# Kernel optimization log

Measured on AMD Instinct MI355X. Metric: run time of the kernel, lower is better.

## Reference

```python
import jax, jax.numpy as jnp
import numpy as np

NUM_HEADS = 8
OUT_FEATS = 64
TOPK_T = 10          # settings['T']
NEG_INF = -9e15

N_NODES = 8192
IN_FEATS = 512
N_EDGES = 262144  # avg degree 32


def setup_inputs() -> dict:
    key = jax.random.key(0)
    k1, k2, k3, k4, k5 = jax.random.split(key, 5)
    feat = jax.random.normal(k1, (N_NODES, IN_FEATS), jnp.float32)
    # xavier-ish scale for the fc weight [H*D, in_feats]
    fc_weight = jax.random.normal(k2, (NUM_HEADS * OUT_FEATS, IN_FEATS), jnp.float32) * 0.05
    trans_m = jax.random.uniform(k3, (N_EDGES,), jnp.float32)
    src = jax.random.randint(k4, (N_EDGES,), 0, N_NODES, dtype=jnp.int32)
    dst = jax.random.randint(k5, (N_EDGES,), 0, N_NODES, dtype=jnp.int32)
    return {"feat": feat, "fc_weight": fc_weight, "trans_m": trans_m, "src": src, "dst": dst}


def reference(feat, fc_weight, trans_m, src, dst):
    N = feat.shape[0]
    # fc projection -> [N, H, D]
    feat_src = (feat @ fc_weight.T).reshape(N, NUM_HEADS, OUT_FEATS)
    # per-edge per-head dot-product score (SDDMM; same math as the gathered NxN matmul)
    fs, fd = feat_src[src], feat_src[dst]           # [Ne, H, D]
    e = jnp.einsum('ehd,ehd->eh', fs, fd)           # [Ne, H]
    # sparse attn values = sum over heads of e * trans_m, scattered into dense [N, N]
    vals = (e * trans_m[:, None]).sum(-1)           # [Ne]
    attn_dense = jnp.zeros((N, N), feat.dtype).at[src, dst].add(vals)
    # topk mask per row: threshold = clamp(kth largest, min=0); below -> -9e15
    thresh = jnp.maximum(jax.lax.top_k(attn_dense, TOPK_T)[0][:, -1], 0.0)  # [N]
    masked = jnp.where(attn_dense < thresh[:, None], NEG_INF, attn_dense)
    # attn = masked.T ; gather attn[src, dst] == masked[dst, src]; mask edges where < -100
    cond = masked[dst, src] < -100.0                # [Ne]
    e = jnp.where(cond[:, None], NEG_INF, e)
    # edge_softmax over incoming edges of each dst node
    emax = jax.ops.segment_max(e, dst, num_segments=N)        # [N, H]
    e_exp = jnp.exp(e - emax[dst])                            # [Ne, H]
    esum = jax.ops.segment_sum(e_exp, dst, num_segments=N)    # [N, H]
    a = e_exp / esum[dst]                                     # [Ne, H]
    # u_mul_e + sum aggregation: rst[v] = sum_{(u,v) in E} a * feat_src[u]
    rst = jax.ops.segment_sum(a[:, :, None] * fs, dst, num_segments=N)  # [N, H, D]
    return rst
```

## Files before the change

kernel.cpp:

```cpp
#include <hip/hip_runtime.h>
#include <hip/hip_bf16.h>
#include <math.h>

#define N_NODES 8192
#define IN_FEATS 512
#define N_EDGES 262144
#define NUM_HEADS 8
#define OUT_FEATS 64
#define HD (NUM_HEADS * OUT_FEATS)
#define TOPK 10
#define NEG_INF -9e15f
#define MAXD 128
#define EID_MASK 0x3FFFF

__device__ __forceinline__ int swz(int row, int k4) {
  return k4 ^ (4 * (((row & 7) ^ ((row >> 3) & 7)) & 7));
}

__global__ __launch_bounds__(512, 2) void gemm_nt(const float* __restrict__ A,
                                                  const float* __restrict__ B,
                                                  float* __restrict__ C,
                                                  ushort* __restrict__ C16) {
  __shared__ char smem[65536];
  int tid = threadIdx.x;
  int sub = tid >> 8;
  int stid = tid & 255;
  int tx = stid & 15, ty = stid >> 4;
  int brow = blockIdx.x * 128, bcol = blockIdx.y * 128;
  int kbase = sub * 256;

  float (*Asub)[32] = (float(*)[32])(smem + sub * 16384);
  float (*Bsub)[32] = (float(*)[32])(smem + 32768 + sub * 16384);

  int sr = stid >> 1;
  int skc = (stid & 1) * 8;
  const float* gA = A + (size_t)(brow + sr) * IN_FEATS + kbase + skc;
  const float* gB = B + (size_t)(bcol + sr) * IN_FEATS + kbase + skc;
  int w0 = swz(sr, skc), w1 = swz(sr, skc + 4);

  float acc[8][8];
#pragma unroll
  for (int i = 0; i < 8; i++)
#pragma unroll
    for (int j = 0; j < 8; j++) acc[i][j] = 0.f;

  float4 ra0 = *(const float4*)gA;
  float4 ra1 = *(const float4*)(gA + 4);
  float4 rb0 = *(const float4*)gB;
  float4 rb1 = *(const float4*)(gB + 4);

  const int NT = 16;
  for (int t = 0; t < NT; ++t) {
    __syncthreads();
    *(float4*)&Asub[sr][w0] = ra0; *(float4*)&Asub[sr][w1] = ra1;
    *(float4*)&Bsub[sr][w0] = rb0; *(float4*)&Bsub[sr][w1] = rb1;
    if (t + 1 < NT) {
      const float* pA = gA + (t + 1) * 16;
      const float* pB = gB + (t + 1) * 16;
      ra0 = *(const float4*)pA; ra1 = *(const float4*)(pA + 4);
      rb0 = *(const float4*)pB; rb1 = *(const float4*)(pB + 4);
    }
    __syncthreads();
#pragma unroll
    for (int g = 0; g < 4; ++g) {
      float4 av[8], bv[8];
#pragma unroll
      for (int i = 0; i < 8; i++) {
        int r = ty * 8 + i;
        av[i] = *(const float4*)&Asub[r][swz(r, g * 4)];
      }
#pragma unroll
      for (int j = 0; j < 8; j++) {
        int c = tx * 8 + j;
        bv[j] = *(const float4*)&Bsub[c][swz(c, g * 4)];
      }
#pragma unroll
      for (int i = 0; i < 8; i++)
#pragma unroll
        for (int j = 0; j < 8; j++) {
          acc[i][j] = fmaf(av[i].x, bv[j].x, acc[i][j]);
          acc[i][j] = fmaf(av[i].y, bv[j].y, acc[i][j]);
          acc[i][j] = fmaf(av[i].z, bv[j].z, acc[i][j]);
          acc[i][j] = fmaf(av[i].w, bv[j].w, acc[i][j]);
        }
    }
  }

  float (*xch)[33] = (float(*)[33])smem;
  __syncthreads();
#pragma unroll
  for (int r = 0; r < 2; ++r) {
    if (sub == 1) {
#pragma unroll
      for (int k = 0; k < 32; ++k) {
        int idx = r * 32 + k;
        xch[stid][k] = acc[idx >> 3][idx & 7];
      }
    }
    __syncthreads();
    if (sub == 0) {
#pragma unroll
      for (int k = 0; k < 32; ++k) {
        int idx = r * 32 + k;
        acc[idx >> 3][idx & 7] += xch[stid][k];
      }
    }
    __syncthreads();
  }

  if (sub == 0) {
#pragma unroll
    for (int i = 0; i < 8; i++) {
      int row = brow + ty * 8 + i;
      float* cp = C + (size_t)row * HD + bcol + tx * 8;
      *(float4*)cp = make_float4(acc[i][0], acc[i][1], acc[i][2], acc[i][3]);
      *(float4*)(cp + 4) = make_float4(acc[i][4], acc[i][5], acc[i][6], acc[i][7]);
      ushort u[8];
#pragma unroll
      for (int j = 0; j < 8; j++) u[j] = __bfloat16_as_ushort(__float2bfloat16(acc[i][j]));
      uint4 q;
      q.x = (unsigned)u[0] | ((unsigned)u[1] << 16);
      q.y = (unsigned)u[2] | ((unsigned)u[3] << 16);
      q.z = (unsigned)u[4] | ((unsigned)u[5] << 16);
      q.w = (unsigned)u[6] | ((unsigned)u[7] << 16);
      *(uint4*)(C16 + (size_t)row * HD + bcol + tx * 8) = q;
    }
  }
}

__global__ __launch_bounds__(256) void histo(const int* __restrict__ src, const int* __restrict__ dst,
                                             int* __restrict__ cnt_s, int* __restrict__ cnt_d) {
  int e = blockIdx.x * blockDim.x + threadIdx.x;
  if (e < N_EDGES) {
    atomicAdd(&cnt_s[src[e]], 1);
    atomicAdd(&cnt_d[dst[e]], 1);
  }
}

__global__ __launch_bounds__(1024) void scan2(const int* __restrict__ cnt_s, const int* __restrict__ cnt_d,
                                              int* __restrict__ rp_s, int* __restrict__ rp_d) {
  __shared__ int ls[1024];
  const int* cnt = blockIdx.x ? cnt_d : cnt_s;
  int* rp = blockIdx.x ? rp_d : rp_s;
  int t = threadIdx.x;
  int base = t * 8;
  int v[8]; int s = 0;
#pragma unroll
  for (int i = 0; i < 8; i++) { v[i] = cnt[base + i]; s += v[i]; }
  ls[t] = s;
  __syncthreads();
  for (int off = 1; off < 1024; off <<= 1) {
    int x = (t >= off) ? ls[t - off] : 0;
    __syncthreads();
    ls[t] += x;
    __syncthreads();
  }
  int excl = (t == 0) ? 0 : ls[t - 1];
#pragma unroll
  for (int i = 0; i < 8; i++) { rp[base + i] = excl; excl += v[i]; }
  if (t == 1023) rp[N_NODES] = excl;
}

__global__ __launch_bounds__(256) void scatter_csr(const int* __restrict__ src, const int* __restrict__ dst,
                                                   const int* __restrict__ rp_s, const int* __restrict__ rp_d,
                                                   int* __restrict__ fill_s, int* __restrict__ fill_d,
                                                   int* __restrict__ cs, int* __restrict__ cd) {
  int e = blockIdx.x * blockDim.x + threadIdx.x;
  if (e < N_EDGES) {
    int p = rp_s[src[e]] + atomicAdd(&fill_s[src[e]], 1);
    cs[p] = e;
    int q = rp_d[dst[e]] + atomicAdd(&fill_d[dst[e]], 1);
    cd[q] = e;
  }
}

__global__ __launch_bounds__(256) void sort_rows_bitonic(const int* __restrict__ rp_s,
                                                         const int* __restrict__ rp_d,
                                                         const int* __restrict__ dst,
                                                         int* __restrict__ cs, int* __restrict__ cd,
                                                         int* __restrict__ keys_s) {
  int wave = (blockIdx.x * blockDim.x + threadIdx.x) >> 6;
  int lane = threadIdx.x & 63;
  bool is_s = wave < N_NODES;
  int r = is_s ? wave : wave - N_NODES;
  const int* rp = is_s ? rp_s : rp_d;
  int b = rp[r], e2 = rp[r + 1];
  int len = e2 - b; if (len > 128) len = 128;

  int x0 = 0x7FFFFFFF, x1 = 0x7FFFFFFF;
  if (lane < len) {
    int e = is_s ? cs[b + lane] : cd[b + lane];
    x0 = is_s ? ((dst[e] << 18) | e) : e;
  }
  if (lane + 64 < len) {
    int e = is_s ? cs[b + lane + 64] : cd[b + lane + 64];
    x1 = is_s ? ((dst[e] << 18) | e) : e;
  }

  for (int s = 2; s <= 64; s <<= 1) {
    bool asc1 = ((64 & s) == 0);
    for (int d = s >> 1; d >= 1; d >>= 1) {
      {
        int y = __shfl_xor(x0, d);
        bool keepmin = (((lane & d) == 0) == ((lane & s) == 0));
        x0 = keepmin ? min(x0, y) : max(x0, y);
      }
      {
        int y = __shfl_xor(x1, d);
        bool asc = asc1 ? ((lane & s) == 0) : false;
        bool keepmin = (((lane & d) == 0) == asc);
        x1 = keepmin ? min(x1, y) : max(x1, y);
      }
    }
  }
  { int lo = min(x0, x1), hi = max(x0, x1); x0 = lo; x1 = hi; }
  for (int d = 32; d >= 1; d >>= 1) {
    {
      int y = __shfl_xor(x0, d);
      bool keepmin = ((lane & d) == 0);
      x0 = keepmin ? min(x0, y) : max(x0, y);
    }
    {
      int y = __shfl_xor(x1, d);
      bool keepmin = ((lane & d) == 0);
      x1 = keepmin ? min(x1, y) : max(x1, y);
    }
  }

  if (lane < len) {
    if (is_s) { cs[b + lane] = x0 & EID_MASK; keys_s[b + lane] = x0; }
    else cd[b + lane] = x0;
  }
  if (lane + 64 < len) {
    if (is_s) { cs[b + lane + 64] = x1 & EID_MASK; keys_s[b + lane + 64] = x1; }
    else cd[b + lane + 64] = x1;
  }
}

__global__ __launch_bounds__(256) void edge_scores_row(const float* __restrict__ fsrc,
                                                       const int* __restrict__ dst,
                                                       const float* __restrict__ trans,
                                                       const int* __restrict__ rp_s,
                                                       const int* __restrict__ cs,
                                                       float* __restrict__ escore, float* __restrict__ val) {
  int wave = (blockIdx.x * blockDim.x + threadIdx.x) >> 6;
  int lane = threadIdx.x & 63;
  if (wave >= N_NODES) return;
  int b = rp_s[wave], e2 = rp_s[wave + 1];
  if (b == e2) return;
  const float4* ps = (const float4*)(fsrc + (size_t)wave * HD) + lane * 2;
  float4 s0 = ps[0], s1 = ps[1];
  int head = lane >> 3;
  bool leader = (lane & 7) == 0;
  for (int i = b; i < e2; i++) {
    int e = cs[i];
    int d = dst[e];
    const float4* pd = (const float4*)(fsrc + (size_t)d * HD) + lane * 2;
    float4 d0 = pd[0], d1 = pd[1];
    float dot = s0.x * d0.x + s0.y * d0.y + s0.z * d0.z + s0.w * d0.w
              + s1.x * d1.x + s1.y * d1.y + s1.z * d1.z + s1.w * d1.w;
    dot += __shfl_xor(dot, 1);
    dot += __shfl_xor(dot, 2);
    dot += __shfl_xor(dot, 4);
    if (leader) escore[(size_t)e * 8 + head] = dot;
    float x = leader ? dot * trans[e] : 0.f;
    x += __shfl_xor(x, 8);
    x += __shfl_xor(x, 16);
    x += __shfl_xor(x, 32);
    if (lane == 0) val[e] = x;
  }
}

__global__ __launch_bounds__(256) void topk_wave(const int* __restrict__ rp_s,
                                                 const int* __restrict__ keys_s,
                                                 const float* __restrict__ val,
                                                 float* __restrict__ aval,
                                                 float* __restrict__ thresh) {
  int wave = (blockIdx.x * blockDim.x + threadIdx.x) >> 6;
  int lane = threadIdx.x & 63;
  if (wave >= N_NODES) return;
  int b = rp_s[wave], e2 = rp_s[wave + 1];
  int len = e2 - b; if (len > 128) len = 128;
  float c[2];
#pragma unroll
  for (int k = 0; k < 2; k++) {
    int i = lane + 64 * k;
    float cv = 0.f;
    if (i < len) {
      int key = keys_s[b + i];
      int d = key >> 18;
      int prevd = (i == 0) ? -1 : (keys_s[b + i - 1] >> 18);
      if (d != prevd) {
        float s = val[key & EID_MASK];
        for (int j = i + 1; j < len; j++) {
          int kj = keys_s[b + j];
          if ((kj >> 18) != d) break;
          s += val[kj & EID_MASK];
        }
        cv = s;
        aval[b + i] = s;
      } else {
        aval[b + i] = 0.f;
      }
    }
    c[k] = cv;
  }
  float t10 = 0.f;
  for (int t = 0; t < 10; t++) {
    float m = fmaxf(c[0], c[1]);
#pragma unroll
    for (int off = 1; off < 64; off <<= 1) m = fmaxf(m, __shfl_xor(m, off));
    if (m <= 0.f) { t10 = 0.f; break; }
    t10 = m;
    if (t == 9) break;
    unsigned long long b0 = __ballot(c[0] == m);
    if (b0) {
      int l = __ffsll(b0) - 1;
      if (lane == l) c[0] = -1e30f;
    } else {
      unsigned long long b1 = __ballot(c[1] == m);
      int l = __ffsll(b1) - 1;
      if (lane == l) c[1] = -1e30f;
    }
  }
  if (lane == 0) thresh[wave] = fmaxf(t10, 0.f);
}

__global__ __launch_bounds__(256) void cond_edges(const int* __restrict__ src, const int* __restrict__ dst,
                                                  const int* __restrict__ rp_s,
                                                  const int* __restrict__ keys_s,
                                                  const float* __restrict__ aval,
                                                  const float* __restrict__ thresh,
                                                  unsigned char* __restrict__ cond) {
  int e = blockIdx.x * blockDim.x + threadIdx.x;
  if (e >= N_EDGES) return;
  int s = src[e], d = dst[e];
  int lo = rp_s[d], hi = rp_s[d + 1];
  int end = hi;
  int target = s << 18;
  while (lo < hi) {
    int mid = (lo + hi) >> 1;
    if (keys_s[mid] < target) lo = mid + 1; else hi = mid;
  }
  float a = 0.f;
  if (lo < end && (keys_s[lo] >> 18) == s) a = aval[lo];
  cond[e] = (a < thresh[d]) ? 1 : 0;
}

__global__ __launch_bounds__(64) void dst_softmax_agg(const int* __restrict__ rp_d, const int* __restrict__ cd,
                                                      const int* __restrict__ src,
                                                      const unsigned char* __restrict__ cond,
                                                      const float* __restrict__ escore,
                                                      const ushort* __restrict__ fsrc16,
                                                      float* __restrict__ out) {
  __shared__ float p_lds[MAXD * 9];
  __shared__ int u_lds[MAXD];
  int v = blockIdx.x;
  int lane = threadIdx.x;
  int rb = rp_d[v], re = rp_d[v + 1];
  int d = re - rb;
  if (d > MAXD) d = MAXD;

  float sc[2][8];
  float m[8];
#pragma unroll
  for (int h = 0; h < 8; h++) m[h] = -3.0e38f;

#pragma unroll
  for (int k = 0; k < 2; k++) {
    int il = lane + 64 * k;
    if (il < d) {
      int ei = cd[rb + il];
      int u = src[ei];
      u_lds[il] = u;
      bool cmask = cond[ei] != 0;
      const float* sp = escore + (size_t)ei * 8;
      float4 s0 = *(const float4*)sp;
      float4 s1 = *(const float4*)(sp + 4);
      float ss[8] = {s0.x, s0.y, s0.z, s0.w, s1.x, s1.y, s1.z, s1.w};
#pragma unroll
      for (int h = 0; h < 8; h++) {
        float x = cmask ? NEG_INF : ss[h];
        sc[k][h] = x;
        m[h] = fmaxf(m[h], x);
      }
    } else {
#pragma unroll
      for (int h = 0; h < 8; h++) sc[k][h] = -3.0e38f;
    }
  }
#pragma unroll
  for (int off = 1; off < 64; off <<= 1)
#pragma unroll
    for (int h = 0; h < 8; h++) m[h] = fmaxf(m[h], __shfl_xor(m[h], off));

  float z[8];
#pragma unroll
  for (int h = 0; h < 8; h++) z[h] = 0.f;
#pragma unroll
  for (int k = 0; k < 2; k++) {
    int il = lane + 64 * k;
    if (il < d) {
#pragma unroll
      for (int h = 0; h < 8; h++) {
        float p = expf(sc[k][h] - m[h]);
        z[h] += p;
        p_lds[il * 9 + h] = p;
      }
    }
  }
#pragma unroll
  for (int off = 1; off < 64; off <<= 1)
#pragma unroll
    for (int h = 0; h < 8; h++) z[h] += __shfl_xor(z[h], off);

  int myh = lane >> 3;
  float zh = 0.f;
#pragma unroll
  for (int h = 0; h < 8; h++) zh = (h == myh) ? z[h] : zh;
  float invZ = (d > 0) ? (1.0f / zh) : 0.f;

  __syncthreads();

  float acc[8];
#pragma unroll
  for (int j = 0; j < 8; j++) acc[j] = 0.f;
  for (int i = 0; i < d; i++) {
    float w = p_lds[i * 9 + myh] * invZ;
    const ushort* fp = fsrc16 + (size_t)u_lds[i] * HD + lane * 8;
    uint4 q = *(const uint4*)fp;
    acc[0] = fmaf(w, __uint_as_float(q.x << 16), acc[0]);
    acc[1] = fmaf(w, __uint_as_float(q.x & 0xFFFF0000u), acc[1]);
    acc[2] = fmaf(w, __uint_as_float(q.y << 16), acc[2]);
    acc[3] = fmaf(w, __uint_as_float(q.y & 0xFFFF0000u), acc[3]);
    acc[4] = fmaf(w, __uint_as_float(q.z << 16), acc[4]);
    acc[5] = fmaf(w, __uint_as_float(q.z & 0xFFFF0000u), acc[5]);
    acc[6] = fmaf(w, __uint_as_float(q.w << 16), acc[6]);
    acc[7] = fmaf(w, __uint_as_float(q.w & 0xFFFF0000u), acc[7]);
  }
  float* op = out + (size_t)v * HD + lane * 8;
  *(float4*)op = make_float4(acc[0], acc[1], acc[2], acc[3]);
  *(float4*)(op + 4) = make_float4(acc[4], acc[5], acc[6], acc[7]);
}

extern "C" void kernel_launch(void* const* d_in, const int* in_sizes, int n_in,
                              void* d_out, int out_size, void* d_ws, size_t ws_size,
                              hipStream_t stream) {
  const float* feat = (const float*)d_in[0];
  const float* fcw = (const float*)d_in[1];
  const float* trans = (const float*)d_in[2];
  const int* src = (const int*)d_in[3];
  const int* dst = (const int*)d_in[4];
  float* out = (float*)d_out;

  char* ws = (char*)d_ws;
  size_t off = 0;
  auto alloc = [&](size_t bytes) -> void* {
    size_t o = off;
    off = (off + bytes + 255) & ~(size_t)255;
    return (void*)(ws + o);
  };
  float* fsrc = (float*)alloc((size_t)N_NODES * HD * 4);
  ushort* fsrc16 = (ushort*)alloc((size_t)N_NODES * HD * 2);
  float* escore = (float*)alloc((size_t)N_EDGES * 8 * 4);
  float* val = (float*)alloc((size_t)N_EDGES * 4);
  int* cnt = (int*)alloc((size_t)4 * N_NODES * 4);
  int* rp_s = (int*)alloc((size_t)(N_NODES + 1) * 4);
  int* rp_d = (int*)alloc((size_t)(N_NODES + 1) * 4);
  int* cs = (int*)alloc((size_t)N_EDGES * 4);
  int* cd = (int*)alloc((size_t)N_EDGES * 4);
  int* keys_s = (int*)alloc((size_t)N_EDGES * 4);
  float* aval = (float*)alloc((size_t)N_EDGES * 4);
  float* thresh = (float*)alloc((size_t)N_NODES * 4);
  unsigned char* cond = (unsigned char*)alloc((size_t)N_EDGES);
  if (off > ws_size) return;

  int* cnt_s = cnt;
  int* cnt_d = cnt + N_NODES;
  int* fill_s = cnt + 2 * N_NODES;
  int* fill_d = cnt + 3 * N_NODES;

  hipMemsetAsync(cnt, 0, (size_t)4 * N_NODES * 4, stream);
  histo<<<N_EDGES / 256, 256, 0, stream>>>(src, dst, cnt_s, cnt_d);
  scan2<<<2, 1024, 0, stream>>>(cnt_s, cnt_d, rp_s, rp_d);
  scatter_csr<<<N_EDGES / 256, 256, 0, stream>>>(src, dst, rp_s, rp_d, fill_s, fill_d, cs, cd);
  sort_rows_bitonic<<<(2 * N_NODES * 64) / 256, 256, 0, stream>>>(rp_s, rp_d, dst, cs, cd, keys_s);
  gemm_nt<<<dim3(N_NODES / 128, HD / 128), 512, 0, stream>>>(feat, fcw, fsrc, fsrc16);
  edge_scores_row<<<(N_NODES * 64) / 256, 256, 0, stream>>>(fsrc, dst, trans, rp_s, cs, escore, val);
  topk_wave<<<(N_NODES * 64) / 256, 256, 0, stream>>>(rp_s, keys_s, val, aval, thresh);
  cond_edges<<<N_EDGES / 256, 256, 0, stream>>>(src, dst, rp_s, keys_s, aval, thresh, cond);
  dst_softmax_agg<<<N_NODES, 64, 0, stream>>>(rp_d, cd, src, cond, escore, fsrc16, out);
}
```

Measured before the change: 259.8 us.

## Double-buffer GEMM LDS tiles and split edge scoring by destination group

The GEMM now keeps two LDS buffers, so the next K-tile is written while the current one is consumed, leaving one barrier per iteration instead of two. This doubles LDS use to 128KB per block, which can lower occupancy. Edge scoring is split into 8 destination-range groups per source row. The sort kernel computes the group offsets with ballots, and each wave processes the edges of one group, giving more parallelism and better locality of gathered destination rows.

```diff
diff --git a/kernel.cpp b/kernel.cpp
--- a/kernel.cpp
+++ b/kernel.cpp
@@ -12,6 +12,8 @@
 #define NEG_INF -9e15f
 #define MAXD 128
 #define EID_MASK 0x3FFFF
+#define NGRP 8
+#define GRP_SHIFT 10
 
 __device__ __forceinline__ int swz(int row, int k4) {
   return k4 ^ (4 * (((row & 7) ^ ((row >> 3) & 7)) & 7));
@@ -21,7 +23,7 @@
                                                   const float* __restrict__ B,
                                                   float* __restrict__ C,
                                                   ushort* __restrict__ C16) {
-  __shared__ char smem[65536];
+  __shared__ char smem[131072];
   int tid = threadIdx.x;
   int sub = tid >> 8;
   int stid = tid & 255;
@@ -29,8 +31,12 @@
   int brow = blockIdx.x * 128, bcol = blockIdx.y * 128;
   int kbase = sub * 256;
 
-  float (*Asub)[32] = (float(*)[32])(smem + sub * 16384);
-  float (*Bsub)[32] = (float(*)[32])(smem + 32768 + sub * 16384);
+  float (*Ab[2])[32];
+  float (*Bb[2])[32];
+  Ab[0] = (float(*)[32])(smem + (sub * 2 + 0) * 16384);
+  Ab[1] = (float(*)[32])(smem + (sub * 2 + 1) * 16384);
+  Bb[0] = (float(*)[32])(smem + 65536 + (sub * 2 + 0) * 16384);
+  Bb[1] = (float(*)[32])(smem + 65536 + (sub * 2 + 1) * 16384);
 
   int sr = stid >> 1;
   int skc = (stid & 1) * 8;
@@ -48,12 +54,15 @@
   float4 ra1 = *(const float4*)(gA + 4);
   float4 rb0 = *(const float4*)gB;
   float4 rb1 = *(const float4*)(gB + 4);
-
+  {
+    float (*A0)[32] = Ab[0]; float (*B0)[32] = Bb[0];
+    *(float4*)&A0[sr][w0] = ra0; *(float4*)&A0[sr][w1] = ra1;
+    *(float4*)&B0[sr][w0] = rb0; *(float4*)&B0[sr][w1] = rb1;
+  }
+
+  int cur = 0;
   const int NT = 16;
   for (int t = 0; t < NT; ++t) {
-    __syncthreads();
-    *(float4*)&Asub[sr][w0] = ra0; *(float4*)&Asub[sr][w1] = ra1;
-    *(float4*)&Bsub[sr][w0] = rb0; *(float4*)&Bsub[sr][w1] = rb1;
     if (t + 1 < NT) {
       const float* pA = gA + (t + 1) * 16;
       const float* pB = gB + (t + 1) * 16;
@@ -61,18 +70,20 @@
       rb0 = *(const float4*)pB; rb1 = *(const float4*)(pB + 4);
     }
     __syncthreads();
+    float (*Acur)[32] = Ab[cur];
+    float (*Bcur)[32] = Bb[cur];
 #pragma unroll
     for (int g = 0; g < 4; ++g) {
       float4 av[8], bv[8];
 #pragma unroll
       for (int i = 0; i < 8; i++) {
         int r = ty * 8 + i;
-        av[i] = *(const float4*)&Asub[r][swz(r, g * 4)];
+        av[i] = *(const float4*)&Acur[r][swz(r, g * 4)];
       }
 #pragma unroll
       for (int j = 0; j < 8; j++) {
         int c = tx * 8 + j;
-        bv[j] = *(const float4*)&Bsub[c][swz(c, g * 4)];
+        bv[j] = *(const float4*)&Bcur[c][swz(c, g * 4)];
       }
 #pragma unroll
       for (int i = 0; i < 8; i++)
@@ -84,6 +95,13 @@
           acc[i][j] = fmaf(av[i].w, bv[j].w, acc[i][j]);
         }
     }
+    if (t + 1 < NT) {
+      float (*Anx)[32] = Ab[cur ^ 1];
+      float (*Bnx)[32] = Bb[cur ^ 1];
+      *(float4*)&Anx[sr][w0] = ra0; *(float4*)&Anx[sr][w1] = ra1;
+      *(float4*)&Bnx[sr][w0] = rb0; *(float4*)&Bnx[sr][w1] = rb1;
+    }
+    cur ^= 1;
   }
 
   float (*xch)[33] = (float(*)[33])smem;
@@ -178,7 +196,8 @@
                                                          const int* __restrict__ rp_d,
                                                          const int* __restrict__ dst,
                                                          int* __restrict__ cs, int* __restrict__ cd,
-                                                         int* __restrict__ keys_s) {
+                                                         int* __restrict__ keys_s,
+                                                         int* __restrict__ grp_off) {
   int wave = (blockIdx.x * blockDim.x + threadIdx.x) >> 6;
   int lane = threadIdx.x & 63;
   bool is_s = wave < N_NODES;
@@ -235,20 +254,39 @@
     if (is_s) { cs[b + lane + 64] = x1 & EID_MASK; keys_s[b + lane + 64] = x1; }
     else cd[b + lane + 64] = x1;
   }
-}
-
-__global__ __launch_bounds__(256) void edge_scores_row(const float* __restrict__ fsrc,
+
+  if (is_s) {
+    if (lane == 0) grp_off[r * NGRP] = b;
+    if (lane >= 1 && lane < NGRP) {
+      int bound = lane << (GRP_SHIFT + 18);
+      int cnt = __popcll(__ballot(x0 < bound)) + __popcll(__ballot(x1 < bound));
+      grp_off[r * NGRP + lane] = b + cnt;
+    } else {
+      __ballot(x0 < 0); __ballot(x1 < 0);
+    }
+  }
+}
+
+__global__ __launch_bounds__(256) void edge_scores_grp(const float* __restrict__ fsrc,
                                                        const int* __restrict__ dst,
                                                        const float* __restrict__ trans,
                                                        const int* __restrict__ rp_s,
                                                        const int* __restrict__ cs,
+                                                       const int* __restrict__ grp_off,
                                                        float* __restrict__ escore, float* __restrict__ val) {
-  int wave = (blockIdx.x * blockDim.x + threadIdx.x) >> 6;
+  int blk = blockIdx.x;
+  int g = blk & 7;
+  int r = (blk >> 3) * 4 + (threadIdx.x >> 6);
   int lane = threadIdx.x & 63;
-  if (wave >= N_NODES) return;
-  int b = rp_s[wave], e2 = rp_s[wave + 1];
-  if (b == e2) return;
-  const float4* ps = (const float4*)(fsrc + (size_t)wave * HD) + lane * 2;
+  int b = grp_off[r * NGRP + g];
+  int e2 = (g == 7) ? rp_s[r + 1] : grp_off[r * NGRP + g + 1];
+  {
+    int rb = rp_s[r];
+    int cap = rb + 128;
+    if (e2 > cap) e2 = cap;
+  }
+  if (b >= e2) return;
+  const float4* ps = (const float4*)(fsrc + (size_t)r * HD) + lane * 2;
   float4 s0 = ps[0], s1 = ps[1];
   int head = lane >> 3;
   bool leader = (lane & 7) == 0;
@@ -472,6 +510,7 @@
   int* keys_s = (int*)alloc((size_t)N_EDGES * 4);
   float* aval = (float*)alloc((size_t)N_EDGES * 4);
   float* thresh = (float*)alloc((size_t)N_NODES * 4);
+  int* grp_off = (int*)alloc((size_t)N_NODES * NGRP * 4);
   unsigned char* cond = (unsigned char*)alloc((size_t)N_EDGES);
   if (off > ws_size) return;
 
@@ -484,9 +523,9 @@
   histo<<<N_EDGES / 256, 256, 0, stream>>>(src, dst, cnt_s, cnt_d);
   scan2<<<2, 1024, 0, stream>>>(cnt_s, cnt_d, rp_s, rp_d);
   scatter_csr<<<N_EDGES / 256, 256, 0, stream>>>(src, dst, rp_s, rp_d, fill_s, fill_d, cs, cd);
-  sort_rows_bitonic<<<(2 * N_NODES * 64) / 256, 256, 0, stream>>>(rp_s, rp_d, dst, cs, cd, keys_s);
+  sort_rows_bitonic<<<(2 * N_NODES * 64) / 256, 256, 0, stream>>>(rp_s, rp_d, dst, cs, cd, keys_s, grp_off);
   gemm_nt<<<dim3(N_NODES / 128, HD / 128), 512, 0, stream>>>(feat, fcw, fsrc, fsrc16);
-  edge_scores_row<<<(N_NODES * 64) / 256, 256, 0, stream>>>(fsrc, dst, trans, rp_s, cs, escore, val);
+  edge_scores_grp<<<NGRP * (N_NODES / 4), 256, 0, stream>>>(fsrc, dst, trans, rp_s, cs, grp_off, escore, val);
   topk_wave<<<(N_NODES * 64) / 256, 256, 0, stream>>>(rp_s, keys_s, val, aval, thresh);
   cond_edges<<<N_EDGES / 256, 256, 0, stream>>>(src, dst, rp_s, keys_s, aval, thresh, cond);
   dst_softmax_agg<<<N_NODES, 64, 0, stream>>>(rp_d, cd, src, cond, escore, fsrc16, out);
```

After: 976.7 us. +275.9%, slower.
